# Optimization experiments

Hardware: AMD Instinct MI355X
Metric: run time of the kernel (lower is better)

Reference implementation:

```python
import jax, jax.numpy as jnp
import numpy as np

N = 100000   # nodes
E = 1600000  # edges (before self-loops)
H = 128      # in_channels == hidden_channels
G = 64       # graphs in batch


def setup_inputs() -> dict:
    key = jax.random.key(0)
    ks = jax.random.split(key, 12)
    s = 1.0 / np.sqrt(H)
    inp = {
        "x": jax.random.normal(ks[0], (N, H), jnp.float32),
        "edge_weight": jax.random.uniform(ks[1], (E,), jnp.float32),
        "edge_index": jax.random.randint(ks[2], (2, E), 0, N, dtype=jnp.int64),
        "batch": jnp.sort(jax.random.randint(ks[3], (N,), 0, G, dtype=jnp.int64)),
        "W1": jax.random.uniform(ks[4], (H, H), jnp.float32, -s, s),
        "b1": jnp.zeros((H,), jnp.float32),
        "W2": jax.random.uniform(ks[5], (H, H), jnp.float32, -s, s),
        "b2": jnp.zeros((H,), jnp.float32),
        "W3": jax.random.uniform(ks[6], (H, H), jnp.float32, -s, s),
        "b3": jnp.zeros((H,), jnp.float32),
        "lin_w": jax.random.uniform(ks[7], (H, 1), jnp.float32, -s, s),
        "lin_b": jax.random.uniform(ks[8], (1,), jnp.float32, -s, s),
    }
    return inp


def reference(x, edge_weight, W1, b1, W2, b2, W3, b3, lin_w, lin_b, edge_index, batch):
    # PyG GCNConv with add_self_loops=True, symmetric normalization.
    loops = jnp.arange(N, dtype=edge_index.dtype)
    row = jnp.concatenate([edge_index[0], loops])  # source
    col = jnp.concatenate([edge_index[1], loops])  # target
    ew = jnp.concatenate([edge_weight, jnp.ones((N,), edge_weight.dtype)])

    deg = jax.ops.segment_sum(ew, col, num_segments=N)          # in-degree (weighted)
    safe = jnp.where(deg > 0, deg, 1.0)
    dinv = jnp.where(deg > 0, jax.lax.rsqrt(safe), 0.0)
    norm = dinv[row] * ew * dinv[col]                            # [E+N]

    def conv(h, W, b):
        h = h @ W                                                # [N,H] dense transform
        msg = h[row] * norm[:, None]                             # gather + scale
        return jax.ops.segment_sum(msg, col, num_segments=N) + b # scatter-add

    h = jax.nn.relu(conv(x, W1, b1))
    h = jax.nn.relu(conv(h, W2, b2))
    h = jax.nn.relu(conv(h, W3, b3))

    # global_mean_pool over graph ids
    sums = jax.ops.segment_sum(h, batch, num_segments=G)         # [G,H]
    cnts = jax.ops.segment_sum(jnp.ones((N,), h.dtype), batch, num_segments=G)
    pooled = sums / jnp.maximum(cnts, 1.0)[:, None]
    # dropout is identity at inference
    return pooled @ lin_w + lin_b                                # [G,1]
```

## Files before the change

### kernel.cpp

```cpp
#include <hip/hip_runtime.h>
#include <stdint.h>

#define N_NODES 100000
#define N_EDGES 1600000
#define HDIM    128
#define G_GRAPHS 64
#define NTOT (N_EDGES + N_NODES)
#define SCAN_NB ((N_NODES + 2047) / 2048)
#define PSLOTS 64
#define NSTRIPS (N_NODES / 16)
#define NTB 512
#define NDB8 ((N_EDGES + 2047) / 2048)
#define PSTR 8

static_assert(N_NODES % 16 == 0, "tile/agg");
static_assert(SCAN_NB <= 64, "scan fixup single wave");

typedef __attribute__((ext_vector_type(8))) short bf16x8;
typedef __attribute__((ext_vector_type(4))) float f32x4;
typedef __attribute__((ext_vector_type(2))) float f32x2;

__device__ __forceinline__ uint32_t f2bf(float x) {
    uint32_t b = __float_as_uint(x);
    return (b + 0x7FFFu + ((b >> 16) & 1u)) >> 16;
}
__device__ __forceinline__ uint32_t pack2(float lo, float hi) {
    return f2bf(lo) | (f2bf(hi) << 16);
}

#define FXSCALE 1099511627776.0f

__global__ void k_wswz(const float* __restrict__ Wb, const float* __restrict__ Wc,
                       uint16_t* __restrict__ dst) {
    int gi = blockIdx.x * 256 + threadIdx.x;
    int w = gi >> 14, idx = gi & 16383;
    const float* src = (w == 0) ? Wb : Wc;
    int k = idx >> 7, n = idx & 127;
    int kc = k >> 5, kq = (k >> 3) & 3, j = k & 7;
    int nt = n >> 4, nl = n & 15;
    dst[w * 16384 + (((kc * 8 + nt) * 64) + kq * 16 + nl) * 8 + j] = (uint16_t)f2bf(src[idx]);
}

__global__ void k_scan1(const unsigned long long* __restrict__ packed,
                        int* __restrict__ cnt, float* __restrict__ dinv,
                        int* __restrict__ partial) {
    int tid = threadIdx.x;
    int base = blockIdx.x * 2048 + tid * 8;
    int s = 0;
#pragma unroll
    for (int j = 0; j < 8; j++) {
        int i = base + j;
        if (i < N_NODES) {
            unsigned long long pk = packed[(size_t)i * PSTR];
            int c = (int)(pk >> 48);
            float deg = (float)(pk & ((1ULL << 48) - 1)) * (1.0f / FXSCALE);
            cnt[i] = c;
            dinv[i] = 1.0f / sqrtf(deg + 1.0f);
            s += c + 1;
        }
    }
    for (int off = 32; off; off >>= 1) s += __shfl_down(s, off);
    __shared__ int sw[4];
    if ((tid & 63) == 0) sw[tid >> 6] = s;
    __syncthreads();
    if (tid == 0) partial[blockIdx.x] = sw[0] + sw[1] + sw[2] + sw[3];
}

__global__ void k_scan3(const int* __restrict__ cnt, const int* __restrict__ partial,
                        int* __restrict__ offs) {
    __shared__ int bbase[SCAN_NB];
    int tid = threadIdx.x;
    if (tid < 64) {
        int v = (tid < SCAN_NB) ? partial[tid] : 0;
        int orig = v;
        for (int off = 1; off < 64; off <<= 1) {
            int u = __shfl_up(v, off);
            if (tid >= off) v += u;
        }
        if (tid < SCAN_NB) bbase[tid] = v - orig;
    }
    int base = blockIdx.x * 2048 + tid * 8;
    int vals[8];
    int tsum = 0;
#pragma unroll
    for (int j = 0; j < 8; j++) {
        int i = base + j;
        vals[j] = (i < N_NODES) ? cnt[i] + 1 : 0;
        tsum += vals[j];
    }
    __shared__ int s[256];
    s[tid] = tsum;
    __syncthreads();
    for (int off = 1; off < 256; off <<= 1) {
        int v = 0;
        if (tid >= off) v = s[tid - off];
        __syncthreads();
        s[tid] += v;
        __syncthreads();
    }
    int run = bbase[blockIdx.x] + s[tid] - tsum;
#pragma unroll
    for (int j = 0; j < 8; j++) {
        int i = base + j;
        if (i < N_NODES) offs[i] = run;
        run += vals[j];
    }
}

__global__ void k_fill(const int* __restrict__ ei, const float* __restrict__ ew,
                       const float* __restrict__ dinv, const int* __restrict__ offs,
                       const int* __restrict__ cnt, const uint16_t* __restrict__ seq,
                       int2* __restrict__ csr) {
    int e = blockIdx.x * 256 + threadIdx.x;
    if (e < N_EDGES) {
        int src = ei[e];
        int dst = ei[N_EDGES + e];
        float nrm = dinv[src] * ew[e] * dinv[dst];
        int p = offs[dst] + (int)seq[e];
        csr[p] = make_int2(src, __float_as_int(nrm));
    } else if (e < NTOT) {
        int i = e - N_EDGES;
        float d = dinv[i];
        int p = offs[i] + cnt[i];
        csr[p] = make_int2(i, __float_as_int(d * d));
    }
}

__device__ __forceinline__ bf16x8 load_row_f32(const float* p) {
    float4 a = ((const float4*)p)[0];
    float4 b = ((const float4*)p)[1];
    union { uint32_t u[4]; bf16x8 v; } c;
    c.u[0] = pack2(a.x, a.y); c.u[1] = pack2(a.z, a.w);
    c.u[2] = pack2(b.x, b.y); c.u[3] = pack2(b.z, b.w);
    return c.v;
}

__device__ __forceinline__ void transform_body_l1(int tb, int nTB, int tid,
                                                  const float* __restrict__ hin,
                                                  const float* __restrict__ Wg,
                                                  uint32_t* __restrict__ t,
                                                  uint16_t* Wf) {
    for (int idx = tid; idx < 16384; idx += 256) {
        int k = idx >> 7, n = idx & 127;
        int kc = k >> 5, kq = (k >> 3) & 3, j = k & 7;
        int nt = n >> 4, nl = n & 15;
        Wf[(((kc * 8 + nt) * 64) + kq * 16 + nl) * 8 + j] = (uint16_t)f2bf(Wg[idx]);
    }
    __syncthreads();
    const bf16x8* Wfrag = (const bf16x8*)Wf;
    int lane = tid & 63;
    int quad = lane >> 4;
    int mrow = lane & 15;
    int gwave = tb * 4 + (tid >> 6);
    int nwaves = nTB * 4;
    for (int strip = gwave; strip < NSTRIPS; strip += nwaves) {
        const float* hrow = hin + ((size_t)(strip * 16 + mrow)) * 128 + quad * 8;
        bf16x8 A0 = load_row_f32(hrow);
        bf16x8 A1 = load_row_f32(hrow + 32);
        bf16x8 A2 = load_row_f32(hrow + 64);
        bf16x8 A3 = load_row_f32(hrow + 96);
        f32x4 acc[8];
#pragma unroll
        for (int nt = 0; nt < 8; nt++) {
            f32x4 a = {0.f, 0.f, 0.f, 0.f};
            a = __builtin_amdgcn_mfma_f32_16x16x32_bf16(A0, Wfrag[(0 * 8 + nt) * 64 + lane], a, 0, 0, 0);
            a = __builtin_amdgcn_mfma_f32_16x16x32_bf16(A1, Wfrag[(1 * 8 + nt) * 64 + lane], a, 0, 0, 0);
            a = __builtin_amdgcn_mfma_f32_16x16x32_bf16(A2, Wfrag[(2 * 8 + nt) * 64 + lane], a, 0, 0, 0);
            a = __builtin_amdgcn_mfma_f32_16x16x32_bf16(A3, Wfrag[(3 * 8 + nt) * 64 + lane], a, 0, 0, 0);
            acc[nt] = a;
        }
#pragma unroll
        for (int nt = 0; nt < 8; nt++) {
#pragma unroll
            for (int r = 0; r < 4; r++) {
                float v = acc[nt][r];
                float nb = __shfl_xor(v, 1);
                int s16 = __builtin_amdgcn_cvt_pk_fp8_f32(v, nb, 0, false);
                int hi  = __shfl_xor(s16, 2);
                if (!(lane & 3)) {
                    int orow = strip * 16 + quad * 4 + r;
                    int oc = (nt * 16 + mrow) >> 2;
                    t[(size_t)orow * 32 + oc] = (uint32_t)(s16 & 0xffff) | ((uint32_t)hi << 16);
                }
            }
        }
    }
}

__global__ __launch_bounds__(256) void k_deg_transform(
        const int* __restrict__ ei, const float* __restrict__ ew,
        unsigned long long* __restrict__ packed, uint16_t* __restrict__ seq,
        const float* __restrict__ x, const float* __restrict__ Wg,
        uint32_t* __restrict__ t) {
    __shared__ uint16_t Wf[16384];
    int bi = blockIdx.x;
    int q5 = bi / 5, r5 = bi % 5;
    int tq = q5 * 2 + r5;
    bool isT = (r5 < 2) && (tq < NTB);
    if (isT) {
        transform_body_l1(tq, NTB, threadIdx.x, x, Wg, t, Wf);
    } else {
        int nTbef = q5 * 2 + (r5 < 2 ? r5 : 2);
        if (nTbef > NTB) nTbef = NTB;
        int db = bi - nTbef;
        int e0 = db * 2048 + threadIdx.x;
        int dstv[8]; float ewv[8];
#pragma unroll
        for (int k = 0; k < 8; k++) {
            int e = e0 + k * 256;
            if (e < N_EDGES) {
                dstv[k] = ei[N_EDGES + e];
                ewv[k] = ew[e];
            } else {
                dstv[k] = -1;
                ewv[k] = 0.f;
            }
        }
        unsigned long long olds[8];
#pragma unroll
        for (int k = 0; k < 8; k++) {
            if (dstv[k] >= 0) {
                unsigned long long pk = (1ULL << 48) | (unsigned long long)(ewv[k] * FXSCALE);
                olds[k] = atomicAdd(&packed[(size_t)dstv[k] * PSTR], pk);
            }
        }
#pragma unroll
        for (int k = 0; k < 8; k++) {
            int e = e0 + k * 256;
            if (e < N_EDGES) seq[e] = (uint16_t)(olds[k] >> 48);
        }
    }
}

__device__ __forceinline__ void aggregate_node(const uint2* __restrict__ t2,
        const int2* __restrict__ csr, int beg, int num, int ql, int grp,
        f32x4& a0, f32x4& a1) {
#define ACCUM(vv, ww) { \
    f32x2 lo0 = __builtin_amdgcn_cvt_pk_f32_fp8((int)vv.x, false); \
    f32x2 hi0 = __builtin_amdgcn_cvt_pk_f32_fp8((int)vv.x, true);  \
    f32x2 lo1 = __builtin_amdgcn_cvt_pk_f32_fp8((int)vv.y, false); \
    f32x2 hi1 = __builtin_amdgcn_cvt_pk_f32_fp8((int)vv.y, true);  \
    a0.x += ww * lo0.x; a0.y += ww * lo0.y; a0.z += ww * hi0.x; a0.w += ww * hi0.y; \
    a1.x += ww * lo1.x; a1.y += ww * lo1.y; a1.z += ww * hi1.x; a1.w += ww * hi1.y; }
    int2 m0 = make_int2(0, 0), m1 = make_int2(0, 0);
    if (ql < num) m0 = csr[beg + ql];
    if (ql + 16 < num) m1 = csr[beg + 16 + ql];
    float mw0 = __int_as_float(m0.y), mw1 = __int_as_float(m1.y);
    int rem = num < 32 ? num : 32;
    int j = 0;
    for (; j + 8 <= rem; j += 8) {
        int   msrc = (j < 16) ? m0.x : m1.x;
        float mw   = (j < 16) ? mw0  : mw1;
        int jj = j & 15;
        int s0 = __shfl(msrc, grp | (jj + 0)), s1 = __shfl(msrc, grp | (jj + 1));
        int s2 = __shfl(msrc, grp | (jj + 2)), s3 = __shfl(msrc, grp | (jj + 3));
        int s4 = __shfl(msrc, grp | (jj + 4)), s5 = __shfl(msrc, grp | (jj + 5));
        int s6 = __shfl(msrc, grp | (jj + 6)), s7 = __shfl(msrc, grp | (jj + 7));
        float w0 = __shfl(mw, grp | (jj + 0)), w1 = __shfl(mw, grp | (jj + 1));
        float w2 = __shfl(mw, grp | (jj + 2)), w3 = __shfl(mw, grp | (jj + 3));
        float w4 = __shfl(mw, grp | (jj + 4)), w5 = __shfl(mw, grp | (jj + 5));
        float w6 = __shfl(mw, grp | (jj + 6)), w7 = __shfl(mw, grp | (jj + 7));
        uint2 v0 = t2[(size_t)s0 * 16 + ql];
        uint2 v1 = t2[(size_t)s1 * 16 + ql];
        uint2 v2 = t2[(size_t)s2 * 16 + ql];
        uint2 v3 = t2[(size_t)s3 * 16 + ql];
        uint2 v4 = t2[(size_t)s4 * 16 + ql];
        uint2 v5 = t2[(size_t)s5 * 16 + ql];
        uint2 v6 = t2[(size_t)s6 * 16 + ql];
        uint2 v7 = t2[(size_t)s7 * 16 + ql];
        ACCUM(v0, w0) ACCUM(v1, w1) ACCUM(v2, w2) ACCUM(v3, w3)
        ACCUM(v4, w4) ACCUM(v5, w5) ACCUM(v6, w6) ACCUM(v7, w7)
    }
    for (; j < rem; j++) {
        int   msrc = (j < 16) ? m0.x : m1.x;
        float mws  = (j < 16) ? mw0  : mw1;
        int   src = __shfl(msrc, grp | (j & 15));
        float w   = __shfl(mws, grp | (j & 15));
        uint2 v = t2[(size_t)src * 16 + ql];
        ACCUM(v, w)
    }
    for (int base = 32; base < num; base += 16) {
        int rem2 = num - base; if (rem2 > 16) rem2 = 16;
        int2 my = make_int2(0, 0);
        if (ql < rem2) my = csr[beg + base + ql];
        int   msrc = my.x;
        float mw   = __int_as_float(my.y);
        int j2 = 0;
        for (; j2 + 8 <= rem2; j2 += 8) {
            int s0 = __shfl(msrc, grp | (j2 + 0)), s1 = __shfl(msrc, grp | (j2 + 1));
            int s2 = __shfl(msrc, grp | (j2 + 2)), s3 = __shfl(msrc, grp | (j2 + 3));
            int s4 = __shfl(msrc, grp | (j2 + 4)), s5 = __shfl(msrc, grp | (j2 + 5));
            int s6 = __shfl(msrc, grp | (j2 + 6)), s7 = __shfl(msrc, grp | (j2 + 7));
            float w0 = __shfl(mw, grp | (j2 + 0)), w1 = __shfl(mw, grp | (j2 + 1));
            float w2 = __shfl(mw, grp | (j2 + 2)), w3 = __shfl(mw, grp | (j2 + 3));
            float w4 = __shfl(mw, grp | (j2 + 4)), w5 = __shfl(mw, grp | (j2 + 5));
            float w6 = __shfl(mw, grp | (j2 + 6)), w7 = __shfl(mw, grp | (j2 + 7));
            uint2 v0 = t2[(size_t)s0 * 16 + ql];
            uint2 v1 = t2[(size_t)s1 * 16 + ql];
            uint2 v2 = t2[(size_t)s2 * 16 + ql];
            uint2 v3 = t2[(size_t)s3 * 16 + ql];
            uint2 v4 = t2[(size_t)s4 * 16 + ql];
            uint2 v5 = t2[(size_t)s5 * 16 + ql];
            uint2 v6 = t2[(size_t)s6 * 16 + ql];
            uint2 v7 = t2[(size_t)s7 * 16 + ql];
            ACCUM(v0, w0) ACCUM(v1, w1) ACCUM(v2, w2) ACCUM(v3, w3)
            ACCUM(v4, w4) ACCUM(v5, w5) ACCUM(v6, w6) ACCUM(v7, w7)
        }
        for (; j2 < rem2; j2++) {
            int   src = __shfl(msrc, grp | j2);
            float w   = __shfl(mw, grp | j2);
            uint2 v = t2[(size_t)src * 16 + ql];
            ACCUM(v, w)
        }
    }
#undef ACCUM
}

__global__ __launch_bounds__(256) void k_agg_tr(
        const uint32_t* __restrict__ tin, const int* __restrict__ offs,
        const int* __restrict__ cnt, const int2* __restrict__ csr,
        const float* __restrict__ bias, const bf16x8* __restrict__ Wfrag,
        uint32_t* __restrict__ tout) {
    __shared__ uint32_t ht[16 * 16 * 4];
    int tid = threadIdx.x;
    int lane = tid & 63;
    int ql = lane & 15;
    int grp = lane & 48;
    int row = (tid >> 6) * 4 + (lane >> 4);
    int node = blockIdx.x * 16 + row;
    int beg = offs[node];
    int num = cnt[node] + 1;
    const uint2* t2 = (const uint2*)tin;
    f32x4 a0 = {0.f, 0.f, 0.f, 0.f};
    f32x4 a1 = {0.f, 0.f, 0.f, 0.f};
    aggregate_node(t2, csr, beg, num, ql, grp, a0, a1);
    float4 b0 = ((const float4*)bias)[ql * 2];
    float4 b1 = ((const float4*)bias)[ql * 2 + 1];
    a0.x = fmaxf(a0.x + b0.x, 0.f); a0.y = fmaxf(a0.y + b0.y, 0.f);
    a0.z = fmaxf(a0.z + b0.z, 0.f); a0.w = fmaxf(a0.w + b0.w, 0.f);
    a1.x = fmaxf(a1.x + b1.x, 0.f); a1.y = fmaxf(a1.y + b1.y, 0.f);
    a1.z = fmaxf(a1.z + b1.z, 0.f); a1.w = fmaxf(a1.w + b1.w, 0.f);
    {
        int slot = (ql + row) & 15;
        uint32_t* dst = &ht[(row * 16 + slot) * 4];
        dst[0] = pack2(a0.x, a0.y);
        dst[1] = pack2(a0.z, a0.w);
        dst[2] = pack2(a1.x, a1.y);
        dst[3] = pack2(a1.z, a1.w);
    }
    __syncthreads();
    int quad = lane >> 4;
    int m = lane & 15;
    int wid = tid >> 6;
    bf16x8 A[4];
#pragma unroll
    for (int c = 0; c < 4; c++) {
        int sl = (c * 4 + quad + m) & 15;
        A[c] = *(const bf16x8*)&ht[(m * 16 + sl) * 4];
    }
    int strip = blockIdx.x;
#pragma unroll
    for (int u = 0; u < 2; u++) {
        int nt = wid * 2 + u;
        f32x4 a = {0.f, 0.f, 0.f, 0.f};
        a = __builtin_amdgcn_mfma_f32_16x16x32_bf16(A[0], Wfrag[(0 * 8 + nt) * 64 + lane], a, 0, 0, 0);
        a = __builtin_amdgcn_mfma_f32_16x16x32_bf16(A[1], Wfrag[(1 * 8 + nt) * 64 + lane], a, 0, 0, 0);
        a = __builtin_amdgcn_mfma_f32_16x16x32_bf16(A[2], Wfrag[(2 * 8 + nt) * 64 + lane], a, 0, 0, 0);
        a = __builtin_amdgcn_mfma_f32_16x16x32_bf16(A[3], Wfrag[(3 * 8 + nt) * 64 + lane], a, 0, 0, 0);
#pragma unroll
        for (int r = 0; r < 4; r++) {
            float v = a[r];
            float nb = __shfl_xor(v, 1);
            int s16 = __builtin_amdgcn_cvt_pk_fp8_f32(v, nb, 0, false);
            int hi  = __shfl_xor(s16, 2);
            if (!(lane & 3)) {
                int orow = strip * 16 + quad * 4 + r;
                int oc = (nt * 16 + m) >> 2;
                tout[(size_t)orow * 32 + oc] = (uint32_t)(s16 & 0xffff) | ((uint32_t)hi << 16);
            }
        }
    }
}

__global__ void k_agg_pool(const uint32_t* __restrict__ t, const int* __restrict__ offs,
                           const int* __restrict__ cnt, const int2* __restrict__ csr,
                           const float* __restrict__ bias, const float* __restrict__ lw,
                           const int* __restrict__ batch, float* __restrict__ pp) {
    int tid = threadIdx.x;
    int lane = tid & 63;
    int ql = lane & 15;
    int grp = lane & 48;
    int node = blockIdx.x * 16 + (tid >> 6) * 4 + (lane >> 4);
    int beg = offs[node];
    int num = cnt[node] + 1;
    const uint2* t2 = (const uint2*)t;
    f32x4 a0 = {0.f, 0.f, 0.f, 0.f};
    f32x4 a1 = {0.f, 0.f, 0.f, 0.f};
    aggregate_node(t2, csr, beg, num, ql, grp, a0, a1);
    float4 b0 = ((const float4*)bias)[ql * 2];
    float4 b1 = ((const float4*)bias)[ql * 2 + 1];
    a0.x = fmaxf(a0.x + b0.x, 0.f); a0.y = fmaxf(a0.y + b0.y, 0.f);
    a0.z = fmaxf(a0.z + b0.z, 0.f); a0.w = fmaxf(a0.w + b0.w, 0.f);
    a1.x = fmaxf(a1.x + b1.x, 0.f); a1.y = fmaxf(a1.y + b1.y, 0.f);
    a1.z = fmaxf(a1.z + b1.z, 0.f); a1.w = fmaxf(a1.w + b1.w, 0.f);
    float4 w0 = ((const float4*)lw)[ql * 2];
    float4 w1 = ((const float4*)lw)[ql * 2 + 1];
    float d = a0.x * w0.x + a0.y * w0.y + a0.z * w0.z + a0.w * w0.w
            + a1.x * w1.x + a1.y * w1.y + a1.z * w1.z + a1.w * w1.w;
    for (int off = 8; off; off >>= 1) d += __shfl_down(d, off);
    if (ql == 0)
        atomicAdd(&pp[(blockIdx.x & (PSLOTS - 1)) * G_GRAPHS + batch[node]], d);
}

__global__ void k_final(const float* __restrict__ pp, const int* __restrict__ batch,
                        const float* __restrict__ lb, float* __restrict__ out) {
    int g = threadIdx.x;
    float s = 0.f;
#pragma unroll
    for (int k = 0; k < PSLOTS; k++) s += pp[k * G_GRAPHS + g];
    int lo = 0, hi = N_NODES;
    while (lo < hi) { int m = (lo + hi) >> 1; if (batch[m] < g) lo = m + 1; else hi = m; }
    int beg = lo;
    hi = N_NODES;
    while (lo < hi) { int m = (lo + hi) >> 1; if (batch[m] < g + 1) lo = m + 1; else hi = m; }
    float c = fmaxf((float)(lo - beg), 1.0f);
    out[g] = s / c + lb[0];
}

extern "C" void kernel_launch(void* const* d_in, const int* in_sizes, int n_in,
                              void* d_out, int out_size, void* d_ws, size_t ws_size,
                              hipStream_t stream) {
    const float* x   = (const float*)d_in[0];
    const float* ew  = (const float*)d_in[1];
    const int*   ei  = (const int*)d_in[2];
    const int*   bat = (const int*)d_in[3];
    const float* W1  = (const float*)d_in[4];
    const float* b1  = (const float*)d_in[5];
    const float* W2  = (const float*)d_in[6];
    const float* b2  = (const float*)d_in[7];
    const float* W3  = (const float*)d_in[8];
    const float* b3  = (const float*)d_in[9];
    const float* lw  = (const float*)d_in[10];
    const float* lb  = (const float*)d_in[11];
    float* out = (float*)d_out;

    char* w = (char*)d_ws;
    size_t o = 0;
    auto carve = [&](size_t bytes) -> void* {
        void* p = w + o;
        o = (o + bytes + 255) & ~(size_t)255;
        return p;
    };
    unsigned long long* packed = (unsigned long long*)carve((size_t)N_NODES * 8 * PSTR);
    float* pp   = (float*)carve((size_t)PSLOTS * G_GRAPHS * 4);
    char*  zero_end = w + o;
    int*      cnt  = (int*)     carve((size_t)N_NODES * 4);
    float*    dinv = (float*)   carve((size_t)N_NODES * 4);
    int*      offs = (int*)     carve((size_t)N_NODES * 4);
    int*      part = (int*)     carve(64 * 4);
    uint16_t* seq  = (uint16_t*)carve((size_t)N_EDGES * 2);
    int2*     csr  = (int2*)    carve((size_t)NTOT * 8);
    uint32_t* tA   = (uint32_t*)carve((size_t)N_NODES * 128);
    uint32_t* tB   = (uint32_t*)carve((size_t)N_NODES * 128);
    uint16_t* wsz  = (uint16_t*)carve((size_t)2 * 16384 * 2);
    (void)ws_size; (void)in_sizes; (void)n_in; (void)out_size;

    hipMemsetAsync(packed, 0, (size_t)(zero_end - (char*)packed), stream);

    k_wswz<<<128, 256, 0, stream>>>(W2, W3, wsz);
    k_deg_transform<<<NTB + NDB8, 256, 0, stream>>>(ei, ew, packed, seq, x, W1, tA);
    k_scan1<<<SCAN_NB, 256, 0, stream>>>(packed, cnt, dinv, part);
    k_scan3<<<SCAN_NB, 256, 0, stream>>>(cnt, part, offs);
    k_fill<<<(NTOT + 255) / 256, 256, 0, stream>>>(ei, ew, dinv, offs, cnt, seq, csr);

    k_agg_tr<<<NSTRIPS, 256, 0, stream>>>(tA, offs, cnt, csr, b1,
                                          (const bf16x8*)wsz, tB);
    k_agg_tr<<<NSTRIPS, 256, 0, stream>>>(tB, offs, cnt, csr, b2,
                                          (const bf16x8*)(wsz + 16384), tA);
    k_agg_pool<<<NSTRIPS, 256, 0, stream>>>(tA, offs, cnt, csr, b3, lw, bat, pp);

    k_final<<<1, G_GRAPHS, 0, stream>>>(pp, bat, lb, out);
}
```

Measured before the change: 402.3 us.

## Build CSR via bucketed two-pass sort with shared-memory degree atomics

Replaces the global 64-bit atomic degree counting and direct CSR fill with a two-level bucket sort. Edges are first histogrammed into 512-node buckets per block, then scanned and scattered into bucket-contiguous records. A per-bucket kernel then computes degrees, ranks and offsets with shared-memory atomics and writes the CSR locally. The destination-side dinv factor moves out of the edge norm and into the aggregation epilogue, multiplying each node's sum by its own dinv. This removes scattered global atomics and the large strided memset, at the cost of more kernel launches, an extra pass over edge records, and a separate normalisation kernel over the CSR.

```diff
diff --git a/kernel.cpp b/kernel.cpp
--- a/kernel.cpp
+++ b/kernel.cpp
@@ -6,15 +6,16 @@
 #define HDIM    128
 #define G_GRAPHS 64
 #define NTOT (N_EDGES + N_NODES)
-#define SCAN_NB ((N_NODES + 2047) / 2048)
 #define PSLOTS 64
 #define NSTRIPS (N_NODES / 16)
 #define NTB 512
-#define NDB8 ((N_EDGES + 2047) / 2048)
-#define PSTR 8
+#define NDB ((N_EDGES + 2047) / 2048)
+#define BSH 9
+#define NBK ((N_NODES + 511) / 512)
+#define MAXBKT 10240
 
 static_assert(N_NODES % 16 == 0, "tile/agg");
-static_assert(SCAN_NB <= 64, "scan fixup single wave");
+static_assert(N_NODES < (1 << 17), "src fits 17 bits");
 
 typedef __attribute__((ext_vector_type(8))) short bf16x8;
 typedef __attribute__((ext_vector_type(4))) float f32x4;
@@ -39,91 +40,6 @@
     int kc = k >> 5, kq = (k >> 3) & 3, j = k & 7;
     int nt = n >> 4, nl = n & 15;
     dst[w * 16384 + (((kc * 8 + nt) * 64) + kq * 16 + nl) * 8 + j] = (uint16_t)f2bf(src[idx]);
-}
-
-__global__ void k_scan1(const unsigned long long* __restrict__ packed,
-                        int* __restrict__ cnt, float* __restrict__ dinv,
-                        int* __restrict__ partial) {
-    int tid = threadIdx.x;
-    int base = blockIdx.x * 2048 + tid * 8;
-    int s = 0;
-#pragma unroll
-    for (int j = 0; j < 8; j++) {
-        int i = base + j;
-        if (i < N_NODES) {
-            unsigned long long pk = packed[(size_t)i * PSTR];
-            int c = (int)(pk >> 48);
-            float deg = (float)(pk & ((1ULL << 48) - 1)) * (1.0f / FXSCALE);
-            cnt[i] = c;
-            dinv[i] = 1.0f / sqrtf(deg + 1.0f);
-            s += c + 1;
-        }
-    }
-    for (int off = 32; off; off >>= 1) s += __shfl_down(s, off);
-    __shared__ int sw[4];
-    if ((tid & 63) == 0) sw[tid >> 6] = s;
-    __syncthreads();
-    if (tid == 0) partial[blockIdx.x] = sw[0] + sw[1] + sw[2] + sw[3];
-}
-
-__global__ void k_scan3(const int* __restrict__ cnt, const int* __restrict__ partial,
-                        int* __restrict__ offs) {
-    __shared__ int bbase[SCAN_NB];
-    int tid = threadIdx.x;
-    if (tid < 64) {
-        int v = (tid < SCAN_NB) ? partial[tid] : 0;
-        int orig = v;
-        for (int off = 1; off < 64; off <<= 1) {
-            int u = __shfl_up(v, off);
-            if (tid >= off) v += u;
-        }
-        if (tid < SCAN_NB) bbase[tid] = v - orig;
-    }
-    int base = blockIdx.x * 2048 + tid * 8;
-    int vals[8];
-    int tsum = 0;
-#pragma unroll
-    for (int j = 0; j < 8; j++) {
-        int i = base + j;
-        vals[j] = (i < N_NODES) ? cnt[i] + 1 : 0;
-        tsum += vals[j];
-    }
-    __shared__ int s[256];
-    s[tid] = tsum;
-    __syncthreads();
-    for (int off = 1; off < 256; off <<= 1) {
-        int v = 0;
-        if (tid >= off) v = s[tid - off];
-        __syncthreads();
-        s[tid] += v;
-        __syncthreads();
-    }
-    int run = bbase[blockIdx.x] + s[tid] - tsum;
-#pragma unroll
-    for (int j = 0; j < 8; j++) {
-        int i = base + j;
-        if (i < N_NODES) offs[i] = run;
-        run += vals[j];
-    }
-}
-
-__global__ void k_fill(const int* __restrict__ ei, const float* __restrict__ ew,
-                       const float* __restrict__ dinv, const int* __restrict__ offs,
-                       const int* __restrict__ cnt, const uint16_t* __restrict__ seq,
-                       int2* __restrict__ csr) {
-    int e = blockIdx.x * 256 + threadIdx.x;
-    if (e < N_EDGES) {
-        int src = ei[e];
-        int dst = ei[N_EDGES + e];
-        float nrm = dinv[src] * ew[e] * dinv[dst];
-        int p = offs[dst] + (int)seq[e];
-        csr[p] = make_int2(src, __float_as_int(nrm));
-    } else if (e < NTOT) {
-        int i = e - N_EDGES;
-        float d = dinv[i];
-        int p = offs[i] + cnt[i];
-        csr[p] = make_int2(i, __float_as_int(d * d));
-    }
 }
 
 __device__ __forceinline__ bf16x8 load_row_f32(const float* p) {
@@ -187,48 +103,171 @@
     }
 }
 
-__global__ __launch_bounds__(256) void k_deg_transform(
-        const int* __restrict__ ei, const float* __restrict__ ew,
-        unsigned long long* __restrict__ packed, uint16_t* __restrict__ seq,
-        const float* __restrict__ x, const float* __restrict__ Wg,
-        uint32_t* __restrict__ t) {
+__global__ __launch_bounds__(256) void k_tr_count(
+        const int* __restrict__ ei, const float* __restrict__ x,
+        const float* __restrict__ Wg, uint32_t* __restrict__ t,
+        int* __restrict__ partials) {
     __shared__ uint16_t Wf[16384];
     int bi = blockIdx.x;
     int q5 = bi / 5, r5 = bi % 5;
     int tq = q5 * 2 + r5;
     bool isT = (r5 < 2) && (tq < NTB);
+    int tid = threadIdx.x;
     if (isT) {
-        transform_body_l1(tq, NTB, threadIdx.x, x, Wg, t, Wf);
+        transform_body_l1(tq, NTB, tid, x, Wg, t, Wf);
     } else {
         int nTbef = q5 * 2 + (r5 < 2 ? r5 : 2);
         if (nTbef > NTB) nTbef = NTB;
         int db = bi - nTbef;
-        int e0 = db * 2048 + threadIdx.x;
-        int dstv[8]; float ewv[8];
+        int* hist = (int*)Wf;
+        for (int i = tid; i < NBK; i += 256) hist[i] = 0;
+        __syncthreads();
+        int e0 = db * 2048 + tid;
 #pragma unroll
         for (int k = 0; k < 8; k++) {
             int e = e0 + k * 256;
-            if (e < N_EDGES) {
-                dstv[k] = ei[N_EDGES + e];
-                ewv[k] = ew[e];
-            } else {
-                dstv[k] = -1;
-                ewv[k] = 0.f;
-            }
-        }
-        unsigned long long olds[8];
-#pragma unroll
-        for (int k = 0; k < 8; k++) {
-            if (dstv[k] >= 0) {
-                unsigned long long pk = (1ULL << 48) | (unsigned long long)(ewv[k] * FXSCALE);
-                olds[k] = atomicAdd(&packed[(size_t)dstv[k] * PSTR], pk);
-            }
-        }
-#pragma unroll
-        for (int k = 0; k < 8; k++) {
-            int e = e0 + k * 256;
-            if (e < N_EDGES) seq[e] = (uint16_t)(olds[k] >> 48);
-        }
+            if (e < N_EDGES) atomicAdd(&hist[ei[N_EDGES + e] >> BSH], 1);
+        }
+        __syncthreads();
+        for (int i = tid; i < NBK; i += 256) partials[i * NDB + db] = hist[i];
+    }
+}
+
+__global__ void k_bscan(const int* __restrict__ partials, int* __restrict__ blockBase,
+                        int* __restrict__ totals) {
+    int b = blockIdx.x, tid = threadIdx.x;
+    int v[4]; int s = 0;
+#pragma unroll
+    for (int j = 0; j < 4; j++) {
+        int i = tid * 4 + j;
+        v[j] = (i < NDB) ? partials[b * NDB + i] : 0;
+        s += v[j];
+    }
+    __shared__ int sm[256];
+    sm[tid] = s; __syncthreads();
+    for (int off = 1; off < 256; off <<= 1) {
+        int u = 0; if (tid >= off) u = sm[tid - off];
+        __syncthreads(); sm[tid] += u; __syncthreads();
+    }
+    int run = sm[tid] - s;
+#pragma unroll
+    for (int j = 0; j < 4; j++) {
+        int i = tid * 4 + j;
+        if (i < NDB) blockBase[b * NDB + i] = run;
+        run += v[j];
+    }
+    if (tid == 255) totals[b] = sm[255];
+}
+
+__global__ void k_starts(const int* __restrict__ totals, int* __restrict__ bstart) {
+    int tid = threadIdx.x;
+    int v = (tid < NBK) ? totals[tid] : 0;
+    __shared__ int sm[256];
+    sm[tid] = v; __syncthreads();
+    for (int off = 1; off < 256; off <<= 1) {
+        int u = 0; if (tid >= off) u = sm[tid - off];
+        __syncthreads(); sm[tid] += u; __syncthreads();
+    }
+    if (tid < NBK) bstart[tid] = sm[tid] - v;
+    if (tid == 255) bstart[NBK] = sm[255];
+}
+
+__global__ __launch_bounds__(256) void k_scatter(
+        const int* __restrict__ ei, const float* __restrict__ ew,
+        const int* __restrict__ blockBase, const int* __restrict__ bstart,
+        uint2* __restrict__ recs) {
+    __shared__ int hist[NBK];
+    __shared__ int basesh[NBK];
+    int tid = threadIdx.x, db = blockIdx.x;
+    for (int i = tid; i < NBK; i += 256) {
+        hist[i] = 0;
+        basesh[i] = bstart[i] + blockBase[i * NDB + db];
+    }
+    __syncthreads();
+    int e0 = db * 2048 + tid;
+#pragma unroll
+    for (int k = 0; k < 8; k++) {
+        int e = e0 + k * 256;
+        if (e < N_EDGES) {
+            int src = ei[e];
+            int dst = ei[N_EDGES + e];
+            float w = ew[e];
+            int bkt = dst >> BSH;
+            int r = atomicAdd(&hist[bkt], 1);
+            recs[basesh[bkt] + r] =
+                make_uint2((uint32_t)src | ((uint32_t)(dst & 511) << 17),
+                           __float_as_uint(w));
+        }
+    }
+}
+
+__global__ __launch_bounds__(256) void k_build(
+        const uint2* __restrict__ recs, const int* __restrict__ bstart,
+        int* __restrict__ cnt, float* __restrict__ dinv, int* __restrict__ offs,
+        int2* __restrict__ csr) {
+    __shared__ unsigned long long acc[512];
+    __shared__ uint16_t rk[MAXBKT];
+    __shared__ int loff[512];
+    __shared__ int sm[256];
+    int b = blockIdx.x, tid = threadIdx.x;
+    int e0 = bstart[b], ne = bstart[b + 1] - e0;
+    for (int i = tid; i < 512; i += 256) acc[i] = 0ULL;
+    __syncthreads();
+    for (int j = tid; j < ne; j += 256) {
+        uint2 rc = recs[e0 + j];
+        int dl = (rc.x >> 17) & 511;
+        float w = __uint_as_float(rc.y);
+        unsigned long long pk = (1ULL << 48) | (unsigned long long)(w * FXSCALE);
+        unsigned long long old = atomicAdd(&acc[dl], pk);
+        rk[j] = (uint16_t)(old >> 48);
+    }
+    __syncthreads();
+    int nb0 = b << BSH;
+    int nreal = N_NODES - nb0; if (nreal > 512) nreal = 512;
+    int i0 = tid * 2, i1 = tid * 2 + 1;
+    int c0 = (i0 < nreal) ? (int)(acc[i0] >> 48) + 1 : 0;
+    int c1 = (i1 < nreal) ? (int)(acc[i1] >> 48) + 1 : 0;
+    sm[tid] = c0 + c1;
+    __syncthreads();
+    for (int off = 1; off < 256; off <<= 1) {
+        int u = 0; if (tid >= off) u = sm[tid - off];
+        __syncthreads(); sm[tid] += u; __syncthreads();
+    }
+    int run = e0 + nb0 + (sm[tid] - (c0 + c1));
+    loff[i0] = run;
+    loff[i1] = run + c0;
+    if (i0 < nreal) {
+        unsigned long long pk = acc[i0];
+        int c = (int)(pk >> 48);
+        float deg = (float)(pk & ((1ULL << 48) - 1)) * (1.0f / FXSCALE);
+        cnt[nb0 + i0] = c;
+        offs[nb0 + i0] = run;
+        dinv[nb0 + i0] = 1.0f / sqrtf(deg + 1.0f);
+        csr[run + c] = make_int2(nb0 + i0, __float_as_int(1.0f));
+    }
+    if (i1 < nreal) {
+        unsigned long long pk = acc[i1];
+        int c = (int)(pk >> 48);
+        float deg = (float)(pk & ((1ULL << 48) - 1)) * (1.0f / FXSCALE);
+        cnt[nb0 + i1] = c;
+        offs[nb0 + i1] = run + c0;
+        dinv[nb0 + i1] = 1.0f / sqrtf(deg + 1.0f);
+        csr[run + c0 + c] = make_int2(nb0 + i1, __float_as_int(1.0f));
+    }
+    __syncthreads();
+    for (int j = tid; j < ne; j += 256) {
+        uint2 rc = recs[e0 + j];
+        int dl = (rc.x >> 17) & 511;
+        int src = rc.x & 0x1ffff;
+        csr[loff[dl] + rk[j]] = make_int2(src, (int)rc.y);
+    }
+}
+
+__global__ void k_norm(int2* __restrict__ csr, const float* __restrict__ dinv) {
+    int p = blockIdx.x * 256 + threadIdx.x;
+    if (p < NTOT) {
+        int2 c = csr[p];
+        csr[p].y = __float_as_int(__int_as_float(c.y) * dinv[c.x]);
     }
 }
 
@@ -319,8 +358,8 @@
 __global__ __launch_bounds__(256) void k_agg_tr(
         const uint32_t* __restrict__ tin, const int* __restrict__ offs,
         const int* __restrict__ cnt, const int2* __restrict__ csr,
-        const float* __restrict__ bias, const bf16x8* __restrict__ Wfrag,
-        uint32_t* __restrict__ tout) {
+        const float* __restrict__ dinv, const float* __restrict__ bias,
+        const bf16x8* __restrict__ Wfrag, uint32_t* __restrict__ tout) {
     __shared__ uint32_t ht[16 * 16 * 4];
     int tid = threadIdx.x;
     int lane = tid & 63;
@@ -330,16 +369,17 @@
     int node = blockIdx.x * 16 + row;
     int beg = offs[node];
     int num = cnt[node] + 1;
+    float dn = dinv[node];
     const uint2* t2 = (const uint2*)tin;
     f32x4 a0 = {0.f, 0.f, 0.f, 0.f};
     f32x4 a1 = {0.f, 0.f, 0.f, 0.f};
     aggregate_node(t2, csr, beg, num, ql, grp, a0, a1);
     float4 b0 = ((const float4*)bias)[ql * 2];
     float4 b1 = ((const float4*)bias)[ql * 2 + 1];
-    a0.x = fmaxf(a0.x + b0.x, 0.f); a0.y = fmaxf(a0.y + b0.y, 0.f);
-    a0.z = fmaxf(a0.z + b0.z, 0.f); a0.w = fmaxf(a0.w + b0.w, 0.f);
-    a1.x = fmaxf(a1.x + b1.x, 0.f); a1.y = fmaxf(a1.y + b1.y, 0.f);
-    a1.z = fmaxf(a1.z + b1.z, 0.f); a1.w = fmaxf(a1.w + b1.w, 0.f);
+    a0.x = fmaxf(a0.x * dn + b0.x, 0.f); a0.y = fmaxf(a0.y * dn + b0.y, 0.f);
+    a0.z = fmaxf(a0.z * dn + b0.z, 0.f); a0.w = fmaxf(a0.w * dn + b0.w, 0.f);
+    a1.x = fmaxf(a1.x * dn + b1.x, 0.f); a1.y = fmaxf(a1.y * dn + b1.y, 0.f);
+    a1.z = fmaxf(a1.z * dn + b1.z, 0.f); a1.w = fmaxf(a1.w * dn + b1.w, 0.f);
     {
         int slot = (ql + row) & 15;
         uint32_t* dst = &ht[(row * 16 + slot) * 4];
@@ -384,8 +424,9 @@
 
 __global__ void k_agg_pool(const uint32_t* __restrict__ t, const int* __restrict__ offs,
                            const int* __restrict__ cnt, const int2* __restrict__ csr,
-                           const float* __restrict__ bias, const float* __restrict__ lw,
-                           const int* __restrict__ batch, float* __restrict__ pp) {
+                           const float* __restrict__ dinv, const float* __restrict__ bias,
+                           const float* __restrict__ lw, const int* __restrict__ batch,
+                           float* __restrict__ pp) {
     int tid = threadIdx.x;
     int lane = tid & 63;
     int ql = lane & 15;
@@ -393,16 +434,17 @@
     int node = blockIdx.x * 16 + (tid >> 6) * 4 + (lane >> 4);
     int beg = offs[node];
     int num = cnt[node] + 1;
+    float dn = dinv[node];
     const uint2* t2 = (const uint2*)t;
     f32x4 a0 = {0.f, 0.f, 0.f, 0.f};
     f32x4 a1 = {0.f, 0.f, 0.f, 0.f};
     aggregate_node(t2, csr, beg, num, ql, grp, a0, a1);
     float4 b0 = ((const float4*)bias)[ql * 2];
     float4 b1 = ((const float4*)bias)[ql * 2 + 1];
-    a0.x = fmaxf(a0.x + b0.x, 0.f); a0.y = fmaxf(a0.y + b0.y, 0.f);
-    a0.z = fmaxf(a0.z + b0.z, 0.f); a0.w = fmaxf(a0.w + b0.w, 0.f);
-    a1.x = fmaxf(a1.x + b1.x, 0.f); a1.y = fmaxf(a1.y + b1.y, 0.f);
-    a1.z = fmaxf(a1.z + b1.z, 0.f); a1.w = fmaxf(a1.w + b1.w, 0.f);
+    a0.x = fmaxf(a0.x * dn + b0.x, 0.f); a0.y = fmaxf(a0.y * dn + b0.y, 0.f);
+    a0.z = fmaxf(a0.z * dn + b0.z, 0.f); a0.w = fmaxf(a0.w * dn + b0.w, 0.f);
+    a1.x = fmaxf(a1.x * dn + b1.x, 0.f); a1.y = fmaxf(a1.y * dn + b1.y, 0.f);
+    a1.z = fmaxf(a1.z * dn + b1.z, 0.f); a1.w = fmaxf(a1.w * dn + b1.w, 0.f);
     float4 w0 = ((const float4*)lw)[ql * 2];
     float4 w1 = ((const float4*)lw)[ql * 2 + 1];
     float d = a0.x * w0.x + a0.y * w0.y + a0.z * w0.z + a0.w * w0.w
@@ -451,33 +493,36 @@
         o = (o + bytes + 255) & ~(size_t)255;
         return p;
     };
-    unsigned long long* packed = (unsigned long long*)carve((size_t)N_NODES * 8 * PSTR);
-    float* pp   = (float*)carve((size_t)PSLOTS * G_GRAPHS * 4);
-    char*  zero_end = w + o;
-    int*      cnt  = (int*)     carve((size_t)N_NODES * 4);
-    float*    dinv = (float*)   carve((size_t)N_NODES * 4);
-    int*      offs = (int*)     carve((size_t)N_NODES * 4);
-    int*      part = (int*)     carve(64 * 4);
-    uint16_t* seq  = (uint16_t*)carve((size_t)N_EDGES * 2);
-    int2*     csr  = (int2*)    carve((size_t)NTOT * 8);
-    uint32_t* tA   = (uint32_t*)carve((size_t)N_NODES * 128);
-    uint32_t* tB   = (uint32_t*)carve((size_t)N_NODES * 128);
-    uint16_t* wsz  = (uint16_t*)carve((size_t)2 * 16384 * 2);
+    float*    pp     = (float*)carve((size_t)PSLOTS * G_GRAPHS * 4);
+    int*      parts  = (int*)  carve((size_t)NBK * NDB * 4);
+    int*      bbase  = (int*)  carve((size_t)NBK * NDB * 4);
+    int*      totals = (int*)  carve((size_t)NBK * 4);
+    int*      bstart = (int*)  carve((size_t)(NBK + 1) * 4);
+    uint2*    recs   = (uint2*)carve((size_t)N_EDGES * 8);
+    int*      cnt    = (int*)  carve((size_t)N_NODES * 4);
+    float*    dinv   = (float*)carve((size_t)N_NODES * 4);
+    int*      offs   = (int*)  carve((size_t)N_NODES * 4);
+    int2*     csr    = (int2*) carve((size_t)NTOT * 8);
+    uint32_t* tA     = (uint32_t*)carve((size_t)N_NODES * 128);
+    uint32_t* tB     = (uint32_t*)carve((size_t)N_NODES * 128);
+    uint16_t* wsz    = (uint16_t*)carve((size_t)2 * 16384 * 2);
     (void)ws_size; (void)in_sizes; (void)n_in; (void)out_size;
 
-    hipMemsetAsync(packed, 0, (size_t)(zero_end - (char*)packed), stream);
+    hipMemsetAsync(pp, 0, (size_t)PSLOTS * G_GRAPHS * 4, stream);
 
     k_wswz<<<128, 256, 0, stream>>>(W2, W3, wsz);
-    k_deg_transform<<<NTB + NDB8, 256, 0, stream>>>(ei, ew, packed, seq, x, W1, tA);
-    k_scan1<<<SCAN_NB, 256, 0, stream>>>(packed, cnt, dinv, part);
-    k_scan3<<<SCAN_NB, 256, 0, stream>>>(cnt, part, offs);
-    k_fill<<<(NTOT + 255) / 256, 256, 0, stream>>>(ei, ew, dinv, offs, cnt, seq, csr);
-
-    k_agg_tr<<<NSTRIPS, 256, 0, stream>>>(tA, offs, cnt, csr, b1,
+    k_tr_count<<<NTB + NDB, 256, 0, stream>>>(ei, x, W1, tA, parts);
+    k_bscan<<<NBK, 256, 0, stream>>>(parts, bbase, totals);
+    k_starts<<<1, 256, 0, stream>>>(totals, bstart);
+    k_scatter<<<NDB, 256, 0, stream>>>(ei, ew, bbase, bstart, recs);
+    k_build<<<NBK, 256, 0, stream>>>(recs, bstart, cnt, dinv, offs, csr);
+    k_norm<<<(NTOT + 255) / 256, 256, 0, stream>>>(csr, dinv);
+
+    k_agg_tr<<<NSTRIPS, 256, 0, stream>>>(tA, offs, cnt, csr, dinv, b1,
                                           (const bf16x8*)wsz, tB);
-    k_agg_tr<<<NSTRIPS, 256, 0, stream>>>(tB, offs, cnt, csr, b2,
+    k_agg_tr<<<NSTRIPS, 256, 0, stream>>>(tB, offs, cnt, csr, dinv, b2,
                                           (const bf16x8*)(wsz + 16384), tA);
-    k_agg_pool<<<NSTRIPS, 256, 0, stream>>>(tA, offs, cnt, csr, b3, lw, bat, pp);
+    k_agg_pool<<<NSTRIPS, 256, 0, stream>>>(tA, offs, cnt, csr, dinv, b3, lw, bat, pp);
 
     k_final<<<1, G_GRAPHS, 0, stream>>>(pp, bat, lb, out);
 }
```

New measurement: 360.7 us. 10.4% less time.
